# Kernel tuning notes

Measured on AMD Instinct MI355X. Metric: run time of the kernel, lower is better.

The kernel has to match this reference:

```python
import jax, jax.numpy as jnp
import numpy as np

NUM_HEAD = 4
HIDDEN = 128
NEG = 9e15


def _mha(x, maskf, wq, bq, wk, bk, wv, bv, wo, bo):
    # DGN-style multi-head attention: relu on q/k/v projections, mask-multiplied
    # scores with -9e15 fill on masked entries, relu on output projection.
    bs, n, _ = x.shape
    dh = HIDDEN // NUM_HEAD
    def proj(w, b):
        return jax.nn.relu(x @ w.T + b).reshape(bs, n, NUM_HEAD, dh).transpose(0, 2, 1, 3)
    q, k, v = proj(wq, bq), proj(wk, bk), proj(wv, bv)  # [bs,H,n,dh]
    scores = jnp.einsum('bhnd,bhmd->bhnm', q, k) / jnp.sqrt(jnp.asarray(dh, x.dtype))
    m = maskf[:, None]  # [bs,1,n,n]
    scores = scores * m - NEG * (1.0 - m)
    att = jax.nn.softmax(scores, axis=-1)
    out = jnp.einsum('bhnm,bhmd->bhnd', att, v).transpose(0, 2, 1, 3).reshape(bs, n, HIDDEN)
    return jax.nn.relu(out @ wo.T + bo), att


def _gru_cell(xin, h, w_ih, w_hh, b_ih, b_hh):
    gi = xin @ w_ih.T + b_ih  # [N, 3*hidden]
    gh = h @ w_hh.T + b_hh
    i_r, i_z, i_n = jnp.split(gi, 3, axis=-1)
    h_r, h_z, h_n = jnp.split(gh, 3, axis=-1)
    r = jax.nn.sigmoid(i_r + h_r)
    z = jax.nn.sigmoid(i_z + h_z)
    n = jnp.tanh(i_n + r * h_n)
    return (1.0 - z) * n + z * h


def setup_inputs() -> dict:
    key = jax.random.key(0)
    ks = jax.random.split(key, 20)
    bs, n_ant, in_dim, hd, act = 4096, 64, 64, 128, 20
    s = 0.05
    x = jax.random.normal(ks[0], (bs, n_ant, in_dim), jnp.float32)
    mask = jax.random.randint(ks[1], (bs, n_ant, n_ant), 0, 2, jnp.int32)
    eye = jnp.eye(n_ant, dtype=jnp.int32)[None]
    mask = jnp.maximum(mask, eye)  # ensure self-edges so no softmax row is fully masked
    hidden_state = jax.random.normal(ks[2], (bs, n_ant, hd), jnp.float32)
    def w(k, shape):
        return jax.random.normal(k, shape, jnp.float32) * s
    return dict(
        x=x, mask=mask, hidden_state=hidden_state,
        enc_w=w(ks[3], (hd, in_dim)), enc_b=jnp.zeros((hd,), jnp.float32),
        q1_w=w(ks[4], (hd, hd)), q1_b=jnp.zeros((hd,), jnp.float32),
        k1_w=w(ks[5], (hd, hd)), k1_b=jnp.zeros((hd,), jnp.float32),
        v1_w=w(ks[6], (hd, hd)), v1_b=jnp.zeros((hd,), jnp.float32),
        o1_w=w(ks[7], (hd, hd)), o1_b=jnp.zeros((hd,), jnp.float32),
        q2_w=w(ks[8], (hd, hd)), q2_b=jnp.zeros((hd,), jnp.float32),
        k2_w=w(ks[9], (hd, hd)), k2_b=jnp.zeros((hd,), jnp.float32),
        v2_w=w(ks[10], (hd, hd)), v2_b=jnp.zeros((hd,), jnp.float32),
        o2_w=w(ks[11], (hd, hd)), o2_b=jnp.zeros((hd,), jnp.float32),
        gru_w_ih=w(ks[12], (3 * hd, hd)), gru_w_hh=w(ks[13], (3 * hd, hd)),
        gru_b_ih=jnp.zeros((3 * hd,), jnp.float32), gru_b_hh=jnp.zeros((3 * hd,), jnp.float32),
        lin_w=w(ks[14], (act, hd)), lin_b=jnp.zeros((act,), jnp.float32),
    )


def reference(x, mask, hidden_state,
              enc_w, enc_b,
              q1_w, q1_b, k1_w, k1_b, v1_w, v1_b, o1_w, o1_b,
              q2_w, q2_b, k2_w, k2_b, v2_w, v2_b, o2_w, o2_b,
              gru_w_ih, gru_w_hh, gru_b_ih, gru_b_hh,
              lin_w, lin_b):
    bs, n_ant, _ = x.shape
    maskf = mask.astype(x.dtype)
    xe = jax.nn.relu(x @ enc_w.T + enc_b)                     # [bs,n,hidden]
    h1, _ = _mha(xe, maskf, q1_w, q1_b, k1_w, k1_b, v1_w, v1_b, o1_w, o1_b)
    h2, _ = _mha(h1, maskf, q2_w, q2_b, k2_w, k2_b, v2_w, v2_b, o2_w, o2_b)
    h2f = h2.reshape(bs * n_ant, HIDDEN)
    hf = hidden_state.reshape(bs * n_ant, HIDDEN)
    h3 = _gru_cell(h2f, hf, gru_w_ih, gru_w_hh, gru_b_ih, gru_b_hh).reshape(bs, n_ant, HIDDEN)
    qs = h3 @ lin_w.T + lin_b                                 # with_non_linearity=False
    return qs, h3
```

## Files before the change

### kernel.cpp

```cpp
#include <hip/hip_runtime.h>
#include <hip/hip_bf16.h>

typedef unsigned int u32;
typedef unsigned short u16;
typedef unsigned long long u64;

using bf16x8 = __attribute__((ext_vector_type(8))) short;
using f32x4  = __attribute__((ext_vector_type(4))) float;
typedef float f4v __attribute__((ext_vector_type(4)));

#define NUNITS 31
#define WS_BIAS_OFF (NUNITS*8192)
#define NBIAS 1952
#define SCL2 0.25503512f
#define L2E  1.4426950408889634f

__device__ __forceinline__ u32 pk2(float a, float b){
    __hip_bfloat162 h = __float22bfloat162_rn(make_float2(a, b));
    union { __hip_bfloat162 h2; u32 u; } cv; cv.h2 = h; return cv.u;
}
__device__ __forceinline__ float b2f(u16 v){ return __uint_as_float(((u32)v) << 16); }
__device__ __forceinline__ int swch(int chunk, int key){ return (chunk & ~7) | ((chunk ^ key) & 7); }
__device__ __forceinline__ float sigx(float v){
    return __builtin_amdgcn_rcpf(1.f + __builtin_amdgcn_exp2f(-L2E * v));
}

__global__ __launch_bounds__(256) void convert_weights(
    const float* __restrict__ enc_w,
    const float* __restrict__ q1, const float* __restrict__ k1,
    const float* __restrict__ v1, const float* __restrict__ o1,
    const float* __restrict__ q2, const float* __restrict__ k2,
    const float* __restrict__ v2, const float* __restrict__ o2,
    const float* __restrict__ gih, const float* __restrict__ ghh,
    const float* __restrict__ lin,
    const float* __restrict__ enc_b,
    const float* __restrict__ q1b, const float* __restrict__ k1b,
    const float* __restrict__ v1b, const float* __restrict__ o1b,
    const float* __restrict__ q2b, const float* __restrict__ k2b,
    const float* __restrict__ v2b, const float* __restrict__ o2b,
    const float* __restrict__ gbih, const float* __restrict__ gbhh,
    const float* __restrict__ linb,
    u16* __restrict__ dst)
{
    int idx = blockIdx.x*256 + threadIdx.x;
    if (idx < NUNITS*8192){
        int u = idx >> 13, rem = idx & 8191;
        int w = rem >> 11;
        int t = (rem >> 9) & 3;
        int l = (rem >> 3) & 63;
        int e = idx & 7;
        int i = t >> 1, kk = t & 1;
        int oc = (w*2 + i)*16 + (l & 15);
        int kl = kk*32 + (l >> 4)*8 + e;
        float val;
        if (u == 0){
            val = enc_w[oc*64 + kl];
        } else if (u <= 16){
            int v = u - 1; int L = v >> 3; int r8 = v & 7;
            int mat, kh;
            if (r8 < 6){ mat = r8 % 3; kh = r8 / 3; } else { mat = 3; kh = r8 - 6; }
            const float* s;
            if (L == 0){ s = (mat==0)?q1:(mat==1)?k1:(mat==2)?v1:o1; }
            else       { s = (mat==0)?q2:(mat==1)?k2:(mat==2)?v2:o2; }
            val = s[oc*128 + kh*64 + kl];
        } else if (u <= 28){
            int v = u - 17;
            int gate, kh; const float* s;
            if (v < 8){ gate = v & 1; kh = (v >> 1) & 1; s = (v >= 4) ? ghh : gih; }
            else      { int w8 = v - 8; gate = 2; kh = w8 & 1; s = (w8 >= 2) ? ghh : gih; }
            val = s[(gate*128 + oc)*128 + kh*64 + kl];
        } else {
            int kh = u - 29;
            val = (oc < 20) ? lin[oc*128 + kh*64 + kl] : 0.f;
        }
        __hip_bfloat16 hv = __float2bfloat16(val);
        union { __hip_bfloat16 h; u16 us; } cv; cv.h = hv;
        dst[idx] = cv.us;
    } else if (idx < NUNITS*8192 + NBIAS){
        int i = idx - NUNITS*8192;
        float val;
        if      (i < 128)  val = enc_b[i];
        else if (i < 256)  val = q1b[i-128];
        else if (i < 384)  val = k1b[i-256];
        else if (i < 512)  val = v1b[i-384];
        else if (i < 640)  val = o1b[i-512];
        else if (i < 768)  val = q2b[i-640];
        else if (i < 896)  val = k2b[i-768];
        else if (i < 1024) val = v2b[i-896];
        else if (i < 1152) val = o2b[i-1024];
        else if (i < 1536) val = gbih[i-1152];
        else if (i < 1920) val = gbhh[i-1536];
        else if (i < 1940) val = linb[i-1920];
        else               val = 0.f;
        ((float*)(dst + NUNITS*8192))[i] = val;
    }
}

#define BARX() do{ asm volatile("s_waitcnt lgkmcnt(0)" ::: "memory"); \
                   __builtin_amdgcn_s_barrier(); \
                   asm volatile("" ::: "memory"); }while(0)

struct WB { bf16x8 a[4]; };

template<int U>
__device__ __forceinline__ WB load_unit(const u16* Wu, int w, int lane){
    const u16* p = Wu + U*8192 + w*2048 + lane*8;
    WB b;
    b.a[0] = *(const bf16x8*)(p);
    b.a[1] = *(const bf16x8*)(p + 512);
    b.a[2] = *(const bf16x8*)(p + 1024);
    b.a[3] = *(const bf16x8*)(p + 1536);
    return b;
}

#define Z4 ((f32x4){0.f,0.f,0.f,0.f})
#define MFMA(a,b,c) __builtin_amdgcn_mfma_f32_16x16x32_bf16((a),(b),(c),0,0,0)

struct XF { bf16x8 f[4][2]; };

__device__ __forceinline__ void loadX(XF& xf, const u16* X, int kh, int c, int g){
    const int key = c & 7;
    #pragma unroll
    for (int kk = 0; kk < 2; kk++){
        const int pw = (kk*4 + g) ^ key;
        #pragma unroll
        for (int j = 0; j < 4; j++)
            xf.f[j][kk] = *(const bf16x8*)(X + (j*16 + c)*128 + (kh*8 + pw)*8);
    }
}

template<bool FIRST>
__device__ __forceinline__ void wgemmW(const WB& wb, const XF& xf, f32x4 (&acc)[2][4]){
    __builtin_amdgcn_s_setprio(1);
    #pragma unroll
    for (int j = 0; j < 4; j++){
        acc[0][j] = FIRST ? MFMA(wb.a[0], xf.f[j][0], Z4) : MFMA(wb.a[0], xf.f[j][0], acc[0][j]);
        acc[1][j] = FIRST ? MFMA(wb.a[2], xf.f[j][0], Z4) : MFMA(wb.a[2], xf.f[j][0], acc[1][j]);
    }
    #pragma unroll
    for (int j = 0; j < 4; j++){
        acc[0][j] = MFMA(wb.a[1], xf.f[j][1], acc[0][j]);
        acc[1][j] = MFMA(wb.a[3], xf.f[j][1], acc[1][j]);
    }
    __builtin_amdgcn_s_setprio(0);
}

template<bool FIRST>
__device__ __forceinline__ void vgemmW(const WB& wb, const XF& xf, f32x4 (&acc)[4][2]){
    __builtin_amdgcn_s_setprio(1);
    #pragma unroll
    for (int i = 0; i < 4; i++){
        acc[i][0] = FIRST ? MFMA(xf.f[i][0], wb.a[0], Z4) : MFMA(xf.f[i][0], wb.a[0], acc[i][0]);
        acc[i][1] = FIRST ? MFMA(xf.f[i][0], wb.a[2], Z4) : MFMA(xf.f[i][0], wb.a[2], acc[i][1]);
    }
    #pragma unroll
    for (int i = 0; i < 4; i++){
        acc[i][0] = MFMA(xf.f[i][1], wb.a[1], acc[i][0]);
        acc[i][1] = MFMA(xf.f[i][1], wb.a[3], acc[i][1]);
    }
    __builtin_amdgcn_s_setprio(0);
}

template<bool QS>
__device__ __forceinline__ void epiW(f32x4 (&acc)[2][4], float4 bv0, float4 bv1,
                                     u16* dst, int w, int c, int g){
    const int key = c & 7;
    #pragma unroll
    for (int i = 0; i < 2; i++){
        float4 bv = i ? bv1 : bv0;
        const int col0 = (w*2+i)*16 + g*4;
        const int coff = swch(col0>>3, key)*8 + (col0&7);
        #pragma unroll
        for (int j = 0; j < 4; j++){
            int row = j*16 + c;
            float v0 = fmaxf(acc[i][j][0]+bv.x, 0.f);
            float v1 = fmaxf(acc[i][j][1]+bv.y, 0.f);
            float v2 = fmaxf(acc[i][j][2]+bv.z, 0.f);
            float v3 = fmaxf(acc[i][j][3]+bv.w, 0.f);
            if (QS){ v0 *= SCL2; v1 *= SCL2; v2 *= SCL2; v3 *= SCL2; }
            uint2 o; o.x = pk2(v0,v1); o.y = pk2(v2,v3);
            *(uint2*)(dst + row*128 + coff) = o;
        }
    }
}

template<int LAYER>
__device__ __forceinline__ void mha_layer(const u16* Wu,
                                          u16* ACT, u16* QXp, u16* KPp,
                                          const float* wsb, const float* h0, size_t rowbase,
                                          int tid, int w, int lane, int c, int g, const u64* mbits,
                                          WB b_q0, WB b_k0, WB b_v0,
                                          WB& nx0, WB& nx1, WB& nx2)
{
    constexpr int UB = 1 + LAYER*8;
    constexpr int BB = 128 + LAYER*512;
    const int key = c & 7;
    const int col00 = w*32 + g*4;
    const int col01 = col00 + 16;

    XF xf;
    f32x4 accQ[2][4], accK[2][4];
    f32x4 vacc[4][2];

    loadX(xf, ACT, 0, c, g);
    wgemmW<true>(b_q0, xf, accQ);
    WB b_q1 = load_unit<UB+3>(Wu, w, lane);
    wgemmW<true>(b_k0, xf, accK);
    WB b_k1 = load_unit<UB+4>(Wu, w, lane);
    vgemmW<true>(b_v0, xf, vacc);
    WB b_v1 = load_unit<UB+5>(Wu, w, lane);

    loadX(xf, ACT, 1, c, g);
    float4 bq0 = *(const float4*)(wsb + BB + col00);
    float4 bq1 = *(const float4*)(wsb + BB + col01);
    wgemmW<false>(b_q1, xf, accQ);
    WB b_o0 = load_unit<UB+6>(Wu, w, lane);
    epiW<true>(accQ, bq0, bq1, QXp, w, c, g);

    float4 bk0 = *(const float4*)(wsb + BB + 128 + col00);
    float4 bk1 = *(const float4*)(wsb + BB + 128 + col01);
    wgemmW<false>(b_k1, xf, accK);
    WB b_o1 = load_unit<UB+7>(Wu, w, lane);
    epiW<false>(accK, bk0, bk1, KPp, w, c, g);

    float bv0 = wsb[BB + 256 + w*32 + c];
    float bv1 = wsb[BB + 256 + w*32 + 16 + c];
    vgemmW<false>(b_v1, xf, vacc);

    BARX();

    #pragma unroll
    for (int j = 0; j < 2; j++){
        int vrow = w*32 + j*16 + c;
        float bv = j ? bv1 : bv0;
        #pragma unroll
        for (int i = 0; i < 4; i++){
            int kk = i >> 1, p = i & 1;
            float v0 = fmaxf(vacc[i][j][0]+bv, 0.f);
            float v1 = fmaxf(vacc[i][j][1]+bv, 0.f);
            float v2 = fmaxf(vacc[i][j][2]+bv, 0.f);
            float v3 = fmaxf(vacc[i][j][3]+bv, 0.f);
            uint2 o; o.x = pk2(v0,v1); o.y = pk2(v2,v3);
            *(uint2*)(ACT + vrow*64 + swch(kk*4+g, key)*8 + p*4) = o;
        }
    }

    const int h = w;
    f32x4 sc[4][4];
    {
        bf16x8 kf[4];
        #pragma unroll
        for (int kt = 0; kt < 4; kt++)
            kf[kt] = *(const bf16x8*)(KPp + (kt*16 + c)*128 + swch(h*4+g, key)*8);
        __builtin_amdgcn_s_setprio(1);
        #pragma unroll
        for (int qt = 0; qt < 4; qt++){
            bf16x8 qf = *(const bf16x8*)(QXp + (qt*16 + c)*128 + swch(h*4+g, key)*8);
            #pragma unroll
            for (int kt = 0; kt < 4; kt++)
                sc[qt][kt] = MFMA(kf[kt], qf, Z4);
        }
        __builtin_amdgcn_s_setprio(0);
    }

    f4v hr[8];
    if (LAYER == 1){
        const float* hp = h0 + (rowbase + (tid>>2))*128 + (tid&3)*32;
        #pragma unroll
        for (int t = 0; t < 8; t++)
            hr[t] = __builtin_nontemporal_load((const f4v*)(hp + t*4));
    }

    {
        u32 pp[4][4][2];
        float inv[4];
        #pragma unroll
        for (int qt = 0; qt < 4; qt++){
            u64 mb = mbits[qt];
            float sum = 0.f;
            #pragma unroll
            for (int kt = 0; kt < 4; kt++)
                #pragma unroll
                for (int r = 0; r < 4; r++){
                    float s = ((mb >> (kt*16 + g*4 + r)) & 1ull) ? sc[qt][kt][r] : -1e30f;
                    float e = __builtin_amdgcn_exp2f(s);
                    sc[qt][kt][r] = e; sum += e;
                }
            sum += __shfl_xor(sum, 16);
            sum += __shfl_xor(sum, 32);
            inv[qt] = __builtin_amdgcn_rcpf(sum);
            #pragma unroll
            for (int kt = 0; kt < 4; kt++){
                pp[qt][kt][0] = pk2(sc[qt][kt][0], sc[qt][kt][1]);
                pp[qt][kt][1] = pk2(sc[qt][kt][2], sc[qt][kt][3]);
            }
        }
        #pragma unroll
        for (int dt = 0; dt < 2; dt++){
            f32x4 pa[4];
            #pragma unroll
            for (int kk = 0; kk < 2; kk++){
                bf16x8 vt = *(const bf16x8*)(ACT + (h*32 + dt*16 + c)*64 + ((kk*4+g)^key)*8);
                __builtin_amdgcn_s_setprio(1);
                #pragma unroll
                for (int qt = 0; qt < 4; qt++){
                    union { u32 u4[4]; bf16x8 v8; } bbv;
                    bbv.u4[0]=pp[qt][kk*2][0];   bbv.u4[1]=pp[qt][kk*2][1];
                    bbv.u4[2]=pp[qt][kk*2+1][0]; bbv.u4[3]=pp[qt][kk*2+1][1];
                    pa[qt] = (kk == 0) ? MFMA(vt, bbv.v8, Z4) : MFMA(vt, bbv.v8, pa[qt]);
                }
                __builtin_amdgcn_s_setprio(0);
            }
            #pragma unroll
            for (int qt = 0; qt < 4; qt++){
                int col = h*32 + dt*16 + g*4;
                float iv = inv[qt];
                uint2 o; o.x = pk2(pa[qt][0]*iv, pa[qt][1]*iv); o.y = pk2(pa[qt][2]*iv, pa[qt][3]*iv);
                *(uint2*)(QXp + (qt*16 + c)*128 + swch(col>>3, key)*8 + (col&7)) = o;
            }
        }
    }

    BARX();

    if (LAYER == 1){
        int hrow = tid >> 2, seg = tid & 3;
        #pragma unroll
        for (int cc = 0; cc < 4; cc++){
            int p = seg*4 + cc;
            int ps = (p & 8) | ((p ^ (hrow & 7)) & 7);
            f4v fa = hr[cc*2], fb = hr[cc*2+1];
            uint4 o; o.x = pk2(fa.x,fa.y); o.y = pk2(fa.z,fa.w);
            o.z = pk2(fb.x,fb.y); o.w = pk2(fb.z,fb.w);
            *(uint4*)(KPp + hrow*128 + ps*8) = o;
        }
    }

    f32x4 acc[2][4];
    loadX(xf, QXp, 0, c, g);
    wgemmW<true>(b_o0, xf, acc);
    nx0 = load_unit<UB+8>(Wu, w, lane);
    nx1 = load_unit<UB+9>(Wu, w, lane);
    loadX(xf, QXp, 1, c, g);
    float4 bo0 = *(const float4*)(wsb + BB + 384 + col00);
    float4 bo1 = *(const float4*)(wsb + BB + 384 + col01);
    wgemmW<false>(b_o1, xf, acc);
    nx2 = load_unit<UB+10>(Wu, w, lane);
    epiW<false>(acc, bo0, bo1, ACT, w, c, g);

    BARX();
}

__global__ __launch_bounds__(256, 2) void drgn_pipe(
    const float* __restrict__ x, const int* __restrict__ maskg,
    const float* __restrict__ h0, const u16* __restrict__ W16,
    float* __restrict__ out_qs, float* __restrict__ out_h3)
{
    __shared__ __align__(16) u16 SMEM[24576];
    u16* ACT = SMEM;
    u16* QXp = SMEM + 8192;
    u16* KPp = SMEM + 16384;

    const int tid = threadIdx.x;
    const int w = tid >> 6, lane = tid & 63;
    const int c = lane & 15, g = lane >> 4;
    const int key = c & 7;
    const size_t rowbase = (size_t)blockIdx.x * 64;
    const u16* Wu = W16;
    const float* wsb = (const float*)(W16 + WS_BIAS_OFF);
    const int col00 = w*32 + g*4;
    const int col01 = col00 + 16;

    u64* MrowT = (u64*)KPp;
    #pragma unroll 4
    for (int rr = 0; rr < 16; rr++){
        int row = w*16 + rr;
        int mv = __builtin_nontemporal_load(maskg + (rowbase + row)*64 + lane);
        u64 bits = __ballot(mv != 0);
        if (lane == 0) MrowT[row] = bits;
    }
    for (int i = tid; i < 512; i += 256){
        int row = i >> 3, p = i & 7;
        int lc = (p ^ (row & 7)) & 7;
        const float* sp = x + (rowbase + row)*64 + lc*8;
        f4v f0 = __builtin_nontemporal_load((const f4v*)sp);
        f4v f1 = __builtin_nontemporal_load((const f4v*)(sp + 4));
        uint4 o; o.x = pk2(f0.x,f0.y); o.y = pk2(f0.z,f0.w);
        o.z = pk2(f1.x,f1.y); o.w = pk2(f1.z,f1.w);
        *(uint4*)(QXp + row*128 + p*8) = o;
    }
    WB b_enc = load_unit<0>(Wu, w, lane);
    WB n0 = load_unit<1>(Wu, w, lane);
    WB n1 = load_unit<2>(Wu, w, lane);
    WB n2 = load_unit<3>(Wu, w, lane);
    __syncthreads();
    u64 mbits[4];
    #pragma unroll
    for (int qt = 0; qt < 4; qt++) mbits[qt] = MrowT[qt*16 + c];

    {
        XF xf;
        f32x4 acc[2][4];
        float4 b0 = *(const float4*)(wsb + col00);
        float4 b1 = *(const float4*)(wsb + col01);
        loadX(xf, QXp, 0, c, g);
        wgemmW<true>(b_enc, xf, acc);
        epiW<false>(acc, b0, b1, ACT, w, c, g);
    }
    BARX();

    mha_layer<0>(Wu, ACT, QXp, KPp, wsb, h0, rowbase, tid, w, lane, c, g, mbits,
                 n0, n1, n2, n0, n1, n2);
    mha_layer<1>(Wu, ACT, QXp, KPp, wsb, h0, rowbase, tid, w, lane, c, g, mbits,
                 n0, n1, n2, n0, n1, n2);

    XF xf;
    float rrA[2][4][4], zzA[2][4][4];
    WB g29, g30;
    {
        f32x4 aIr[2][4], aIz[2][4], aHr[2][4], aHz[2][4];
        loadX(xf, ACT, 0, c, g);
        wgemmW<true>(n0, xf, aIr);
        WB g20 = load_unit<20>(Wu, w, lane);
        wgemmW<true>(n1, xf, aIz);
        WB g21 = load_unit<21>(Wu, w, lane);
        loadX(xf, ACT, 1, c, g);
        wgemmW<false>(n2, xf, aIr);
        WB g22 = load_unit<22>(Wu, w, lane);
        wgemmW<false>(g20, xf, aIz);
        WB g23 = load_unit<23>(Wu, w, lane);
        loadX(xf, KPp, 0, c, g);
        wgemmW<true>(g21, xf, aHr);
        WB g24 = load_unit<24>(Wu, w, lane);
        wgemmW<true>(g22, xf, aHz);
        WB g25 = load_unit<25>(Wu, w, lane);
        loadX(xf, KPp, 1, c, g);
        wgemmW<false>(g23, xf, aHr);
        WB g26 = load_unit<26>(Wu, w, lane);
        wgemmW<false>(g24, xf, aHz);
        WB g27 = load_unit<27>(Wu, w, lane);

        float4 bir0 = *(const float4*)(wsb + 1152 + col00);
        float4 bir1 = *(const float4*)(wsb + 1152 + col01);
        float4 bhr0 = *(const float4*)(wsb + 1536 + col00);
        float4 bhr1 = *(const float4*)(wsb + 1536 + col01);
        float4 biz0 = *(const float4*)(wsb + 1152 + 128 + col00);
        float4 biz1 = *(const float4*)(wsb + 1152 + 128 + col01);
        float4 bhz0 = *(const float4*)(wsb + 1536 + 128 + col00);
        float4 bhz1 = *(const float4*)(wsb + 1536 + 128 + col01);
        #pragma unroll
        for (int i = 0; i < 2; i++){
            float4 bir = i ? bir1 : bir0; float4 bhr = i ? bhr1 : bhr0;
            float4 biz = i ? biz1 : biz0; float4 bhz = i ? bhz1 : bhz0;
            #pragma unroll
            for (int j = 0; j < 4; j++)
                #pragma unroll
                for (int r = 0; r < 4; r++){
                    rrA[i][j][r] = sigx(aIr[i][j][r] + (&bir.x)[r] + aHr[i][j][r] + (&bhr.x)[r]);
                    zzA[i][j][r] = sigx(aIz[i][j][r] + (&biz.x)[r] + aHz[i][j][r] + (&bhz.x)[r]);
                }
        }

        f32x4 aIn[2][4], aHn[2][4];
        loadX(xf, ACT, 0, c, g);
        wgemmW<true>(g25, xf, aIn);
        WB g28 = load_unit<28>(Wu, w, lane);
        loadX(xf, ACT, 1, c, g);
        wgemmW<false>(g26, xf, aIn);
        g29 = load_unit<29>(Wu, w, lane);
        loadX(xf, KPp, 0, c, g);
        wgemmW<true>(g27, xf, aHn);
        g30 = load_unit<30>(Wu, w, lane);
        loadX(xf, KPp, 1, c, g);
        wgemmW<false>(g28, xf, aHn);

        float4 bin0 = *(const float4*)(wsb + 1152 + 256 + col00);
        float4 bin1 = *(const float4*)(wsb + 1152 + 256 + col01);
        float4 bhn0 = *(const float4*)(wsb + 1536 + 256 + col00);
        float4 bhn1 = *(const float4*)(wsb + 1536 + 256 + col01);

        BARX();

        #pragma unroll
        for (int i = 0; i < 2; i++){
            float4 bi = i ? bin1 : bin0; float4 bh = i ? bhn1 : bhn0;
            int col0 = w*32 + i*16 + g*4;
            int coff = swch(col0>>3, key)*8 + (col0&7);
            #pragma unroll
            for (int j = 0; j < 4; j++){
                int row = j*16 + c;
                uint2 hv = *(const uint2*)(KPp + row*128 + coff);
                float h0v[4] = { b2f((u16)(hv.x & 0xffffu)), b2f((u16)(hv.x >> 16)),
                                 b2f((u16)(hv.y & 0xffffu)), b2f((u16)(hv.y >> 16)) };
                f4v h3o;
                #pragma unroll
                for (int r = 0; r < 4; r++){
                    float xn = aIn[i][j][r] + (&bi.x)[r] + rrA[i][j][r]*(aHn[i][j][r] + (&bh.x)[r]);
                    float e2 = __builtin_amdgcn_exp2f(-2.f*L2E*fabsf(xn));
                    float th = (1.f - e2)*__builtin_amdgcn_rcpf(1.f + e2);
                    th = (xn >= 0.f) ? th : -th;
                    float zv = zzA[i][j][r];
                    h3o[r] = (1.f - zv)*th + zv*h0v[r];
                }
                uint2 o; o.x = pk2(h3o[0],h3o[1]); o.y = pk2(h3o[2],h3o[3]);
                *(uint2*)(ACT + row*128 + coff) = o;
                __builtin_nontemporal_store(h3o, (f4v*)(out_h3 + (rowbase + row)*128 + col0));
            }
        }
    }
    BARX();

    {
        f32x4 qa[2][4];
        float4 lb0 = (col00 < 20) ? *(const float4*)(wsb + 1920 + col00) : (float4){0.f,0.f,0.f,0.f};
        float4 lb1 = (col01 < 20) ? *(const float4*)(wsb + 1920 + col01) : (float4){0.f,0.f,0.f,0.f};
        loadX(xf, ACT, 0, c, g);
        wgemmW<true>(g29, xf, qa);
        loadX(xf, ACT, 1, c, g);
        wgemmW<false>(g30, xf, qa);

        #pragma unroll
        for (int i = 0; i < 2; i++){
            int col0 = w*32 + i*16 + g*4;
            if (col0 < 20){
                float4 lb = i ? lb1 : lb0;
                #pragma unroll
                for (int j = 0; j < 4; j++){
                    int row = j*16 + c;
                    f4v o;
                    o.x = qa[i][j][0]+lb.x; o.y = qa[i][j][1]+lb.y;
                    o.z = qa[i][j][2]+lb.z; o.w = qa[i][j][3]+lb.w;
                    __builtin_nontemporal_store(o, (f4v*)(out_qs + (rowbase + row)*20 + col0));
                }
            }
        }
    }
}

extern "C" void kernel_launch(void* const* d_in, const int* in_sizes, int n_in,
                              void* d_out, int out_size, void* d_ws, size_t ws_size,
                              hipStream_t stream) {
    const float* x     = (const float*)d_in[0];
    const int*   mask  = (const int*)  d_in[1];
    const float* h0    = (const float*)d_in[2];
    const float* enc_w = (const float*)d_in[3];
    const float* enc_b = (const float*)d_in[4];
    const float* q1_w  = (const float*)d_in[5];  const float* q1_b = (const float*)d_in[6];
    const float* k1_w  = (const float*)d_in[7];  const float* k1_b = (const float*)d_in[8];
    const float* v1_w  = (const float*)d_in[9];  const float* v1_b = (const float*)d_in[10];
    const float* o1_w  = (const float*)d_in[11]; const float* o1_b = (const float*)d_in[12];
    const float* q2_w  = (const float*)d_in[13]; const float* q2_b = (const float*)d_in[14];
    const float* k2_w  = (const float*)d_in[15]; const float* k2_b = (const float*)d_in[16];
    const float* v2_w  = (const float*)d_in[17]; const float* v2_b = (const float*)d_in[18];
    const float* o2_w  = (const float*)d_in[19]; const float* o2_b = (const float*)d_in[20];
    const float* gwih  = (const float*)d_in[21]; const float* gwhh = (const float*)d_in[22];
    const float* gbih  = (const float*)d_in[23]; const float* gbhh = (const float*)d_in[24];
    const float* lin_w = (const float*)d_in[25]; const float* lin_b = (const float*)d_in[26];

    const int bs = in_sizes[0] / (64 * 64);
    float* out_qs = (float*)d_out;
    float* out_h3 = out_qs + (size_t)bs * 64 * 20;
    u16* W16 = (u16*)d_ws;

    const int total = NUNITS*8192 + NBIAS;
    hipLaunchKernelGGL(convert_weights, dim3((total + 255) / 256), dim3(256), 0, stream,
                       enc_w, q1_w, k1_w, v1_w, o1_w, q2_w, k2_w, v2_w, o2_w,
                       gwih, gwhh, lin_w,
                       enc_b, q1_b, k1_b, v1_b, o1_b, q2_b, k2_b, v2_b, o2_b,
                       gbih, gbhh, lin_b, W16);
    hipLaunchKernelGGL(drgn_pipe, dim3(bs), dim3(256), 0, stream,
                       x, mask, h0, W16, out_qs, out_h3);
}
```

Baseline: 313.1 us.

## Ping-pong two shared buffers to cut LDS and raise blocks per CU

Drops shared memory from three 16KB activation buffers to two. Each attention layer now alternates between an input and an output buffer: K is written over the consumed input after a barrier, and the softmax/P computation moves ahead of the V store. Launch bounds go from 2 to 4 blocks per SM so more blocks can be resident. The cost is extra barriers and tighter register budgets, which could cause spills and makes the buffer reuse ordering fragile.

```diff
diff --git a/kernel.cpp b/kernel.cpp
--- a/kernel.cpp
+++ b/kernel.cpp
@@ -186,7 +186,7 @@
 
 template<int LAYER>
 __device__ __forceinline__ void mha_layer(const u16* Wu,
-                                          u16* ACT, u16* QXp, u16* KPp,
+                                          u16* IN, u16* OUT,
                                           const float* wsb, const float* h0, size_t rowbase,
                                           int tid, int w, int lane, int c, int g, const u64* mbits,
                                           WB b_q0, WB b_k0, WB b_v0,
@@ -202,7 +202,7 @@
     f32x4 accQ[2][4], accK[2][4];
     f32x4 vacc[4][2];
 
-    loadX(xf, ACT, 0, c, g);
+    loadX(xf, IN, 0, c, g);
     wgemmW<true>(b_q0, xf, accQ);
     WB b_q1 = load_unit<UB+3>(Wu, w, lane);
     wgemmW<true>(b_k0, xf, accK);
@@ -210,22 +210,75 @@
     vgemmW<true>(b_v0, xf, vacc);
     WB b_v1 = load_unit<UB+5>(Wu, w, lane);
 
-    loadX(xf, ACT, 1, c, g);
+    loadX(xf, IN, 1, c, g);
     float4 bq0 = *(const float4*)(wsb + BB + col00);
     float4 bq1 = *(const float4*)(wsb + BB + col01);
     wgemmW<false>(b_q1, xf, accQ);
     WB b_o0 = load_unit<UB+6>(Wu, w, lane);
-    epiW<true>(accQ, bq0, bq1, QXp, w, c, g);
+    epiW<true>(accQ, bq0, bq1, OUT, w, c, g);
 
     float4 bk0 = *(const float4*)(wsb + BB + 128 + col00);
     float4 bk1 = *(const float4*)(wsb + BB + 128 + col01);
     wgemmW<false>(b_k1, xf, accK);
     WB b_o1 = load_unit<UB+7>(Wu, w, lane);
-    epiW<false>(accK, bk0, bk1, KPp, w, c, g);
 
     float bv0 = wsb[BB + 256 + w*32 + c];
     float bv1 = wsb[BB + 256 + w*32 + 16 + c];
     vgemmW<false>(b_v1, xf, vacc);
+
+    BARX();
+
+    epiW<false>(accK, bk0, bk1, IN, w, c, g);
+
+    const int h = w;
+    f32x4 sc[4][4];
+    {
+        bf16x8 kf[4];
+        #pragma unroll
+        for (int kt = 0; kt < 4; kt++)
+            kf[kt] = *(const bf16x8*)(IN + (kt*16 + c)*128 + swch(h*4+g, key)*8);
+        __builtin_amdgcn_s_setprio(1);
+        #pragma unroll
+        for (int qt = 0; qt < 4; qt++){
+            bf16x8 qf = *(const bf16x8*)(OUT + (qt*16 + c)*128 + swch(h*4+g, key)*8);
+            #pragma unroll
+            for (int kt = 0; kt < 4; kt++)
+                sc[qt][kt] = MFMA(kf[kt], qf, Z4);
+        }
+        __builtin_amdgcn_s_setprio(0);
+    }
+
+    f4v hr[8];
+    if (LAYER == 1){
+        const float* hp = h0 + (rowbase + (tid>>2))*128 + (tid&3)*32;
+        #pragma unroll
+        for (int t = 0; t < 8; t++)
+            hr[t] = __builtin_nontemporal_load((const f4v*)(hp + t*4));
+    }
+
+    u32 pp[4][4][2];
+    float inv[4];
+    #pragma unroll
+    for (int qt = 0; qt < 4; qt++){
+        u64 mb = mbits[qt];
+        float sum = 0.f;
+        #pragma unroll
+        for (int kt = 0; kt < 4; kt++)
+            #pragma unroll
+            for (int r = 0; r < 4; r++){
+                float s = ((mb >> (kt*16 + g*4 + r)) & 1ull) ? sc[qt][kt][r] : -1e30f;
+                float e = __builtin_amdgcn_exp2f(s);
+                sc[qt][kt][r] = e; sum += e;
+            }
+        sum += __shfl_xor(sum, 16);
+        sum += __shfl_xor(sum, 32);
+        inv[qt] = __builtin_amdgcn_rcpf(sum);
+        #pragma unroll
+        for (int kt = 0; kt < 4; kt++){
+            pp[qt][kt][0] = pk2(sc[qt][kt][0], sc[qt][kt][1]);
+            pp[qt][kt][1] = pk2(sc[qt][kt][2], sc[qt][kt][3]);
+        }
+    }
 
     BARX();
 
@@ -241,89 +294,44 @@
             float v2 = fmaxf(vacc[i][j][2]+bv, 0.f);
             float v3 = fmaxf(vacc[i][j][3]+bv, 0.f);
             uint2 o; o.x = pk2(v0,v1); o.y = pk2(v2,v3);
-            *(uint2*)(ACT + vrow*64 + swch(kk*4+g, key)*8 + p*4) = o;
-        }
-    }
-
-    const int h = w;
-    f32x4 sc[4][4];
-    {
-        bf16x8 kf[4];
-        #pragma unroll
-        for (int kt = 0; kt < 4; kt++)
-            kf[kt] = *(const bf16x8*)(KPp + (kt*16 + c)*128 + swch(h*4+g, key)*8);
-        __builtin_amdgcn_s_setprio(1);
-        #pragma unroll
-        for (int qt = 0; qt < 4; qt++){
-            bf16x8 qf = *(const bf16x8*)(QXp + (qt*16 + c)*128 + swch(h*4+g, key)*8);
-            #pragma unroll
-            for (int kt = 0; kt < 4; kt++)
-                sc[qt][kt] = MFMA(kf[kt], qf, Z4);
-        }
-        __builtin_amdgcn_s_setprio(0);
-    }
-
-    f4v hr[8];
-    if (LAYER == 1){
-        const float* hp = h0 + (rowbase + (tid>>2))*128 + (tid&3)*32;
-        #pragma unroll
-        for (int t = 0; t < 8; t++)
-            hr[t] = __builtin_nontemporal_load((const f4v*)(hp + t*4));
-    }
-
-    {
-        u32 pp[4][4][2];
-        float inv[4];
-        #pragma unroll
-        for (int qt = 0; qt < 4; qt++){
-            u64 mb = mbits[qt];
-            float sum = 0.f;
-            #pragma unroll
-            for (int kt = 0; kt < 4; kt++)
-                #pragma unroll
-                for (int r = 0; r < 4; r++){
-                    float s = ((mb >> (kt*16 + g*4 + r)) & 1ull) ? sc[qt][kt][r] : -1e30f;
-                    float e = __builtin_amdgcn_exp2f(s);
-                    sc[qt][kt][r] = e; sum += e;
-                }
-            sum += __shfl_xor(sum, 16);
-            sum += __shfl_xor(sum, 32);
-            inv[qt] = __builtin_amdgcn_rcpf(sum);
-            #pragma unroll
-            for (int kt = 0; kt < 4; kt++){
-                pp[qt][kt][0] = pk2(sc[qt][kt][0], sc[qt][kt][1]);
-                pp[qt][kt][1] = pk2(sc[qt][kt][2], sc[qt][kt][3]);
-            }
-        }
-        #pragma unroll
-        for (int dt = 0; dt < 2; dt++){
-            f32x4 pa[4];
-            #pragma unroll
-            for (int kk = 0; kk < 2; kk++){
-                bf16x8 vt = *(const bf16x8*)(ACT + (h*32 + dt*16 + c)*64 + ((kk*4+g)^key)*8);
-                __builtin_amdgcn_s_setprio(1);
-                #pragma unroll
-                for (int qt = 0; qt < 4; qt++){
-                    union { u32 u4[4]; bf16x8 v8; } bbv;
-                    bbv.u4[0]=pp[qt][kk*2][0];   bbv.u4[1]=pp[qt][kk*2][1];
-                    bbv.u4[2]=pp[qt][kk*2+1][0]; bbv.u4[3]=pp[qt][kk*2+1][1];
-                    pa[qt] = (kk == 0) ? MFMA(vt, bbv.v8, Z4) : MFMA(vt, bbv.v8, pa[qt]);
-                }
-                __builtin_amdgcn_s_setprio(0);
-            }
+            *(uint2*)(OUT + vrow*64 + swch(kk*4+g, key)*8 + p*4) = o;
+        }
+    }
+
+    #pragma unroll
+    for (int dt = 0; dt < 2; dt++){
+        f32x4 pa[4];
+        #pragma unroll
+        for (int kk = 0; kk < 2; kk++){
+            bf16x8 vt = *(const bf16x8*)(OUT + (h*32 + dt*16 + c)*64 + ((kk*4+g)^key)*8);
+            __builtin_amdgcn_s_setprio(1);
             #pragma unroll
             for (int qt = 0; qt < 4; qt++){
-                int col = h*32 + dt*16 + g*4;
-                float iv = inv[qt];
-                uint2 o; o.x = pk2(pa[qt][0]*iv, pa[qt][1]*iv); o.y = pk2(pa[qt][2]*iv, pa[qt][3]*iv);
-                *(uint2*)(QXp + (qt*16 + c)*128 + swch(col>>3, key)*8 + (col&7)) = o;
+                union { u32 u4[4]; bf16x8 v8; } bbv;
+                bbv.u4[0]=pp[qt][kk*2][0];   bbv.u4[1]=pp[qt][kk*2][1];
+                bbv.u4[2]=pp[qt][kk*2+1][0]; bbv.u4[3]=pp[qt][kk*2+1][1];
+                pa[qt] = (kk == 0) ? MFMA(vt, bbv.v8, Z4) : MFMA(vt, bbv.v8, pa[qt]);
             }
+            __builtin_amdgcn_s_setprio(0);
+        }
+        #pragma unroll
+        for (int qt = 0; qt < 4; qt++){
+            int col = h*32 + dt*16 + g*4;
+            float iv = inv[qt];
+            uint2 o; o.x = pk2(pa[qt][0]*iv, pa[qt][1]*iv); o.y = pk2(pa[qt][2]*iv, pa[qt][3]*iv);
+            *(uint2*)(IN + (qt*16 + c)*128 + swch(col>>3, key)*8 + (col&7)) = o;
         }
     }
 
     BARX();
 
+    f32x4 acc[2][4];
+    loadX(xf, IN, 0, c, g);
+    wgemmW<true>(b_o0, xf, acc);
+    loadX(xf, IN, 1, c, g);
+
     if (LAYER == 1){
+        BARX();
         int hrow = tid >> 2, seg = tid & 3;
         #pragma unroll
         for (int cc = 0; cc < 4; cc++){
@@ -332,34 +340,29 @@
             f4v fa = hr[cc*2], fb = hr[cc*2+1];
             uint4 o; o.x = pk2(fa.x,fa.y); o.y = pk2(fa.z,fa.w);
             o.z = pk2(fb.x,fb.y); o.w = pk2(fb.z,fb.w);
-            *(uint4*)(KPp + hrow*128 + ps*8) = o;
-        }
-    }
-
-    f32x4 acc[2][4];
-    loadX(xf, QXp, 0, c, g);
-    wgemmW<true>(b_o0, xf, acc);
-    nx0 = load_unit<UB+8>(Wu, w, lane);
-    nx1 = load_unit<UB+9>(Wu, w, lane);
-    loadX(xf, QXp, 1, c, g);
+            *(uint4*)(IN + hrow*128 + ps*8) = o;
+        }
+    }
+
     float4 bo0 = *(const float4*)(wsb + BB + 384 + col00);
     float4 bo1 = *(const float4*)(wsb + BB + 384 + col01);
     wgemmW<false>(b_o1, xf, acc);
+    nx0 = load_unit<UB+8>(Wu, w, lane);
+    nx1 = load_unit<UB+9>(Wu, w, lane);
     nx2 = load_unit<UB+10>(Wu, w, lane);
-    epiW<false>(acc, bo0, bo1, ACT, w, c, g);
+    epiW<false>(acc, bo0, bo1, OUT, w, c, g);
 
     BARX();
 }
 
-__global__ __launch_bounds__(256, 2) void drgn_pipe(
+__global__ __launch_bounds__(256, 4) void drgn_pipe(
     const float* __restrict__ x, const int* __restrict__ maskg,
     const float* __restrict__ h0, const u16* __restrict__ W16,
     float* __restrict__ out_qs, float* __restrict__ out_h3)
 {
-    __shared__ __align__(16) u16 SMEM[24576];
-    u16* ACT = SMEM;
-    u16* QXp = SMEM + 8192;
-    u16* KPp = SMEM + 16384;
+    __shared__ __align__(16) u16 SMEM[16384];
+    u16* A = SMEM;
+    u16* B = SMEM + 8192;
 
     const int tid = threadIdx.x;
     const int w = tid >> 6, lane = tid & 63;
@@ -371,7 +374,7 @@
     const int col00 = w*32 + g*4;
     const int col01 = col00 + 16;
 
-    u64* MrowT = (u64*)KPp;
+    u64* MrowT = (u64*)B;
     #pragma unroll 4
     for (int rr = 0; rr < 16; rr++){
         int row = w*16 + rr;
@@ -387,7 +390,7 @@
         f4v f1 = __builtin_nontemporal_load((const f4v*)(sp + 4));
         uint4 o; o.x = pk2(f0.x,f0.y); o.y = pk2(f0.z,f0.w);
         o.z = pk2(f1.x,f1.y); o.w = pk2(f1.z,f1.w);
-        *(uint4*)(QXp + row*128 + p*8) = o;
+        *(uint4*)(A + row*128 + p*8) = o;
     }
     WB b_enc = load_unit<0>(Wu, w, lane);
     WB n0 = load_unit<1>(Wu, w, lane);
@@ -403,38 +406,37 @@
         f32x4 acc[2][4];
         float4 b0 = *(const float4*)(wsb + col00);
         float4 b1 = *(const float4*)(wsb + col01);
-        loadX(xf, QXp, 0, c, g);
+        loadX(xf, A, 0, c, g);
         wgemmW<true>(b_enc, xf, acc);
-        epiW<false>(acc, b0, b1, ACT, w, c, g);
+        BARX();
+        epiW<false>(acc, b0, b1, B, w, c, g);
     }
     BARX();
 
-    mha_layer<0>(Wu, ACT, QXp, KPp, wsb, h0, rowbase, tid, w, lane, c, g, mbits,
-                 n0, n1, n2, n0, n1, n2);
-    mha_layer<1>(Wu, ACT, QXp, KPp, wsb, h0, rowbase, tid, w, lane, c, g, mbits,
-                 n0, n1, n2, n0, n1, n2);
+    mha_layer<0>(Wu, B, A, wsb, h0, rowbase, tid, w, lane, c, g, mbits, n0, n1, n2, n0, n1, n2);
+    mha_layer<1>(Wu, A, B, wsb, h0, rowbase, tid, w, lane, c, g, mbits, n0, n1, n2, n0, n1, n2);
 
     XF xf;
     float rrA[2][4][4], zzA[2][4][4];
     WB g29, g30;
     {
         f32x4 aIr[2][4], aIz[2][4], aHr[2][4], aHz[2][4];
-        loadX(xf, ACT, 0, c, g);
+        loadX(xf, B, 0, c, g);
         wgemmW<true>(n0, xf, aIr);
         WB g20 = load_unit<20>(Wu, w, lane);
         wgemmW<true>(n1, xf, aIz);
         WB g21 = load_unit<21>(Wu, w, lane);
-        loadX(xf, ACT, 1, c, g);
+        loadX(xf, B, 1, c, g);
         wgemmW<false>(n2, xf, aIr);
         WB g22 = load_unit<22>(Wu, w, lane);
         wgemmW<false>(g20, xf, aIz);
         WB g23 = load_unit<23>(Wu, w, lane);
-        loadX(xf, KPp, 0, c, g);
+        loadX(xf, A, 0, c, g);
         wgemmW<true>(g21, xf, aHr);
         WB g24 = load_unit<24>(Wu, w, lane);
         wgemmW<true>(g22, xf, aHz);
         WB g25 = load_unit<25>(Wu, w, lane);
-        loadX(xf, KPp, 1, c, g);
+        loadX(xf, A, 1, c, g);
         wgemmW<false>(g23, xf, aHr);
         WB g26 = load_unit<26>(Wu, w, lane);
         wgemmW<false>(g24, xf, aHz);
@@ -462,16 +464,16 @@
         }
 
         f32x4 aIn[2][4], aHn[2][4];
-        loadX(xf, ACT, 0, c, g);
+        loadX(xf, B, 0, c, g);
         wgemmW<true>(g25, xf, aIn);
         WB g28 = load_unit<28>(Wu, w, lane);
-        loadX(xf, ACT, 1, c, g);
+        loadX(xf, B, 1, c, g);
         wgemmW<false>(g26, xf, aIn);
         g29 = load_unit<29>(Wu, w, lane);
-        loadX(xf, KPp, 0, c, g);
+        loadX(xf, A, 0, c, g);
         wgemmW<true>(g27, xf, aHn);
         g30 = load_unit<30>(Wu, w, lane);
-        loadX(xf, KPp, 1, c, g);
+        loadX(xf, A, 1, c, g);
         wgemmW<false>(g28, xf, aHn);
 
         float4 bin0 = *(const float4*)(wsb + 1152 + 256 + col00);
@@ -489,7 +491,7 @@
             #pragma unroll
             for (int j = 0; j < 4; j++){
                 int row = j*16 + c;
-                uint2 hv = *(const uint2*)(KPp + row*128 + coff);
+                uint2 hv = *(const uint2*)(A + row*128 + coff);
                 float h0v[4] = { b2f((u16)(hv.x & 0xffffu)), b2f((u16)(hv.x >> 16)),
                                  b2f((u16)(hv.y & 0xffffu)), b2f((u16)(hv.y >> 16)) };
                 f4v h3o;
@@ -503,7 +505,7 @@
                     h3o[r] = (1.f - zv)*th + zv*h0v[r];
                 }
                 uint2 o; o.x = pk2(h3o[0],h3o[1]); o.y = pk2(h3o[2],h3o[3]);
-                *(uint2*)(ACT + row*128 + coff) = o;
+                *(uint2*)(B + row*128 + coff) = o;
                 __builtin_nontemporal_store(h3o, (f4v*)(out_h3 + (rowbase + row)*128 + col0));
             }
         }
@@ -514,9 +516,9 @@
         f32x4 qa[2][4];
         float4 lb0 = (col00 < 20) ? *(const float4*)(wsb + 1920 + col00) : (float4){0.f,0.f,0.f,0.f};
         float4 lb1 = (col01 < 20) ? *(const float4*)(wsb + 1920 + col01) : (float4){0.f,0.f,0.f,0.f};
-        loadX(xf, ACT, 0, c, g);
+        loadX(xf, B, 0, c, g);
         wgemmW<true>(g29, xf, qa);
-        loadX(xf, ACT, 1, c, g);
+        loadX(xf, B, 1, c, g);
         wgemmW<false>(g30, xf, qa);
 
         #pragma unroll
```

Result: slower. 1.119 ms (+257.4%).
